# Optimization experiments

Hardware: AMD Instinct MI355X
Metric: run time of the kernel (lower is better)

Reference implementation:

```python
import jax, jax.numpy as jnp
import numpy as np
from jax import lax

TAU_REF_HOURS = 1.0
INIT_NOISE_SCALE = 0.01
MAX_GROWTH_RATE = 0.3
B, T, N, D = 2, 64, 512, 256


def setup_inputs() -> dict:
    key = jax.random.key(0)
    ks = jax.random.split(key, 8)
    return {
        "x": jax.random.normal(ks[0], (B, T, N, D), dtype=jnp.float32),
        "dt": jax.random.uniform(ks[1], (B, T), dtype=jnp.float32),
        "eps": jax.random.normal(ks[2], (B, T, N, D), dtype=jnp.float32),
        "u_raw_re": jax.random.normal(ks[3], (D, D), dtype=jnp.float32) * 0.02,
        "u_raw_im": jax.random.normal(ks[4], (D, D), dtype=jnp.float32) * 0.02,
        "lam_re": jax.random.normal(ks[5], (D,), dtype=jnp.float32) * 0.01,
        "lam_im": jax.random.normal(ks[6], (D,), dtype=jnp.float32) * 0.1,
        "noise_raw": jax.random.normal(ks[7], (D,), dtype=jnp.float32) * 0.02,
    }


def reference(x, dt, eps, u_raw_re, u_raw_im, lam_re, lam_im, noise_raw):
    # Unitary basis from QR of complex raw matrix (ComplexSVDTransform._unitary_from_raw)
    u, _ = jnp.linalg.qr(lax.complex(u_raw_re, u_raw_im))  # [D, D] complex

    # encode: x @ conj(u)
    x_enc = jnp.einsum("btnd,de->btne", x.astype(jnp.complex64), jnp.conj(u))

    # effective lambda: lam_re -> -softplus(-lam_re), clamped at -max_growth_rate
    lam_r = jnp.maximum(-jax.nn.softplus(-lam_re), -MAX_GROWTH_RATE)
    lam = lax.complex(lam_r, lam_im)  # [D]

    # continuous decay / forcing operators per (b, t, d)
    exp_arg = (dt / TAU_REF_HOURS)[..., None] * lam  # [B, T, D]
    decay = jnp.exp(exp_arg)
    lam_safe = lam + (1e-8 * jnp.sign(lam_r + 1e-12)).astype(lam.dtype)
    forcing = (decay - 1.0) / lam_safe  # expm1(arg)/lam_safe

    # SDE noise: eps * sqrt(dt) * softplus(noise_raw) * init_noise_scale
    dt_scale = jnp.sqrt(jnp.maximum(dt, 0.0))[:, :, None, None]  # [B,T,1,1]
    n_scale = jax.nn.softplus(noise_raw) * INIT_NOISE_SCALE  # [D]
    noise = eps.astype(jnp.complex64) * (dt_scale * n_scale).astype(jnp.complex64)

    # linear recurrence h_t = decay_t * h_{t-1} + forcing_t * x_enc_t + noise_t
    b_term = forcing[:, :, None, :] * x_enc + noise  # [B,T,N,D]
    a_term = jnp.broadcast_to(decay[:, :, None, :], b_term.shape)

    def combine(e1, e2):
        a1, b1 = e1
        a2, b2 = e2
        return (a2 * a1, a2 * b1 + b2)

    _, h = lax.associative_scan(combine, (a_term, b_term), axis=1)  # [B,T,N,D]

    # decode: h @ u
    y = jnp.einsum("btnd,de->btne", h, u)
    return jnp.stack([y.real, y.imag])  # [2,B,T,N,D] float32
```

## Files before the change

### kernel.cpp

```cpp
#include <hip/hip_runtime.h>
#include <math.h>

#define B_ 2
#define T_ 64
#define N_ 512
#define D_ 256
#define M_ (B_*T_*N_)
#define PLANE ((size_t)M_*D_)

typedef unsigned short u16;
typedef __attribute__((ext_vector_type(8))) short bf16x8;
typedef __attribute__((ext_vector_type(4))) float f32x4;

__device__ __forceinline__ u16 f2bf(float f) {
  union { float f; unsigned u; } cv; cv.f = f;
  unsigned u = cv.u;
  return (u16)((u + 0x7FFFu + ((u >> 16) & 1u)) >> 16);
}
__device__ __forceinline__ float bf2f(u16 h) {
  union { unsigned u; float f; } cv; cv.u = ((unsigned)h) << 16;
  return cv.f;
}

__device__ __forceinline__ float wredsum(float x) {
  x += __uint_as_float(__builtin_amdgcn_update_dpp(0u, __float_as_uint(x), 0x111, 0xf, 0xf, true));
  x += __uint_as_float(__builtin_amdgcn_update_dpp(0u, __float_as_uint(x), 0x112, 0xf, 0xf, true));
  x += __uint_as_float(__builtin_amdgcn_update_dpp(0u, __float_as_uint(x), 0x114, 0xf, 0xf, true));
  x += __uint_as_float(__builtin_amdgcn_update_dpp(0u, __float_as_uint(x), 0x118, 0xf, 0xf, true));
  x += __uint_as_float(__builtin_amdgcn_update_dpp(0u, __float_as_uint(x), 0x142, 0xa, 0xf, true));
  x += __uint_as_float(__builtin_amdgcn_update_dpp(0u, __float_as_uint(x), 0x143, 0xc, 0xf, true));
  return __uint_as_float(__builtin_amdgcn_readlane(__float_as_uint(x), 63));
}
__device__ __forceinline__ float lanebcast(float x, int l) {
  return __uint_as_float(__builtin_amdgcn_readlane(__float_as_uint(x), l));
}

template<int P>
__global__ __launch_bounds__(1024, 1) void qr_megastep(
    const float* __restrict__ ure_raw, const float* __restrict__ uim_raw,
    float2* __restrict__ A, float2* __restrict__ tau)
{
  const int tid = threadIdx.x, lane = tid & 63, w = tid >> 6;
  const int role = blockIdx.x;
  __shared__ float2 sv32[32][256];
  __shared__ float2 sfin[32][256];
  __shared__ float2 snA[2][256];
  __shared__ float2 snB[2][256];
  __shared__ float4 sscalAB[2];
  __shared__ float2 sg[2];
  __shared__ float2 sgp[16];
  __shared__ float2 stau32[32];
  __shared__ float2 stauOut[32];

  constexpr int J0P  = (P > 0) ? 32*(P-1) : 0;
  constexpr int RP   = 256 - J0P;
  constexpr int MCHP = (RP + 63) >> 6;
  constexpr int PIV  = (P == 0) ? 0 : 32;
  constexpr int J0W  = (P == 0) ? 0 : J0P;
  constexpr int RW   = 256 - J0W;
  constexpr int MCHW = (RW + 63) >> 6;

  if constexpr (P == 0) {
    if (role > 0) {
      const int c0 = 32*role;
      const int c = tid & 31, r0 = tid >> 5;
      #pragma unroll
      for (int r8 = 0; r8 < 8; ++r8) {
        int r = r0 + r8*32;
        A[(size_t)(c0+c)*D_ + r] = make_float2(ure_raw[(size_t)r*D_ + c0 + c],
                                               uim_raw[(size_t)r*D_ + c0 + c]);
      }
      return;
    }
  }

  float2 col[2][4];

  if constexpr (P > 0) {
    #pragma unroll
    for (int it = 0; it < 8; ++it) {
      int idx = it*1024 + tid;
      int c = idx >> 8, rr = idx & 255;
      float2 val = make_float2(0.f, 0.f);
      if (rr < RP) val = A[(size_t)(J0P+c)*D_ + J0P + rr];
      sv32[c][rr] = val;
    }
    if (tid < 32) stau32[tid] = tau[J0P + tid];
    const int c0 = (role > 0) ? 32*(P + role) : 32*P;
    #pragma unroll
    for (int lc = 0; lc < 2; ++lc) {
      int cg = c0 + 2*w + lc;
      #pragma unroll
      for (int m = 0; m < 4; ++m) {
        int rr = m*64 + lane;
        col[lc][m] = make_float2(0.f, 0.f);
        if (m < MCHP && rr < RP) col[lc][m] = A[(size_t)cg*D_ + J0P + rr];
      }
    }
    __syncthreads();

    {
      const int ja = 2*w, jb = 2*w + 1;
      float2 va[4], vb[4];
      { float2 rv = sv32[ja][lane];
        va[0] = (lane > ja) ? rv : ((lane == ja) ? make_float2(1.f, 0.f)
                                                 : make_float2(0.f, 0.f)); }
      { float2 rv = sv32[jb][lane];
        vb[0] = (lane > jb) ? rv : ((lane == jb) ? make_float2(1.f, 0.f)
                                                 : make_float2(0.f, 0.f)); }
      #pragma unroll
      for (int m = 1; m < 4; ++m) { va[m] = sv32[ja][m*64 + lane];
                                    vb[m] = sv32[jb][m*64 + lane]; }
      float gr = 0.f, gi = 0.f;
      #pragma unroll
      for (int m = 0; m < 4; ++m) {
        if (m < MCHP) {
          gr += vb[m].x*va[m].x + vb[m].y*va[m].y;
          gi += vb[m].x*va[m].y - vb[m].y*va[m].x;
        }
      }
      gr = wredsum(gr); gi = wredsum(gi);
      if (lane == 0) sgp[w] = make_float2(gr, gi);
    }
    __syncthreads();

    #pragma unroll 2
    for (int m = 0; m < 16; ++m) {
      const int ja = 2*m, jb = 2*m + 1;
      float2 tA = stau32[ja], tB = stau32[jb];
      float2 g = sgp[m];
      float2 vA[4], vB[4];
      { float2 rv = sv32[ja][lane];
        vA[0] = (lane > ja) ? rv : ((lane == ja) ? make_float2(1.f, 0.f)
                                                 : make_float2(0.f, 0.f)); }
      { float2 rv = sv32[jb][lane];
        vB[0] = (lane > jb) ? rv : ((lane == jb) ? make_float2(1.f, 0.f)
                                                 : make_float2(0.f, 0.f)); }
      #pragma unroll
      for (int mm = 1; mm < 4; ++mm) { vA[mm] = sv32[ja][mm*64 + lane];
                                       vB[mm] = sv32[jb][mm*64 + lane]; }
      #pragma unroll
      for (int lc = 0; lc < 2; ++lc) {
        float d1r = 0.f, d1i = 0.f, d2r = 0.f, d2i = 0.f;
        #pragma unroll
        for (int mm = 0; mm < 4; ++mm) {
          if (mm < MCHP) {
            float2 a = col[lc][mm];
            d1r += vA[mm].x*a.x + vA[mm].y*a.y;
            d1i += vA[mm].x*a.y - vA[mm].y*a.x;
            d2r += vB[mm].x*a.x + vB[mm].y*a.y;
            d2i += vB[mm].x*a.y - vB[mm].y*a.x;
          }
        }
        d1r = wredsum(d1r); d1i = wredsum(d1i);
        d2r = wredsum(d2r); d2i = wredsum(d2i);
        float f1r = tA.x*d1r + tA.y*d1i;
        float f1i = tA.x*d1i - tA.y*d1r;
        float d2cr = d2r - (f1r*g.x - f1i*g.y);
        float d2ci = d2i - (f1r*g.y + f1i*g.x);
        float f2r = tB.x*d2cr + tB.y*d2ci;
        float f2i = tB.x*d2ci - tB.y*d2cr;
        #pragma unroll
        for (int mm = 0; mm < 4; ++mm) {
          if (mm < MCHP) {
            col[lc][mm].x -= f1r*vA[mm].x - f1i*vA[mm].y
                           + f2r*vB[mm].x - f2i*vB[mm].y;
            col[lc][mm].y -= f1r*vA[mm].y + f1i*vA[mm].x
                           + f2r*vB[mm].y + f2i*vB[mm].x;
          }
        }
      }
    }

    if (role > 0) {
      #pragma unroll
      for (int lc = 0; lc < 2; ++lc) {
        int cg = 32*(P + role) + 2*w + lc;
        #pragma unroll
        for (int m = 0; m < 4; ++m) {
          int rr = m*64 + lane;
          if (m < MCHP && rr < RP) A[(size_t)cg*D_ + J0P + rr] = col[lc][m];
        }
      }
      return;
    }
    __syncthreads();
  } else {
    #pragma unroll
    for (int lc = 0; lc < 2; ++lc) {
      int cg = 2*w + lc;
      #pragma unroll
      for (int m = 0; m < 4; ++m) {
        int rr = m*64 + lane;
        col[lc][m] = make_float2(ure_raw[(size_t)rr*D_ + cg],
                                 uim_raw[(size_t)rr*D_ + cg]);
      }
    }
  }

  auto derive_pair = [&](float2 (&ca)[4], float2 (&cb)[4], int jlA, int buf) {
    const int prA = PIV + jlA, prB = prA + 1;
    float part = (lane > prA) ? (ca[0].x*ca[0].x + ca[0].y*ca[0].y) : 0.f;
    if (1 < MCHW) part += ca[1].x*ca[1].x + ca[1].y*ca[1].y;
    if (2 < MCHW) part += ca[2].x*ca[2].x + ca[2].y*ca[2].y;
    if (3 < MCHW) part += ca[3].x*ca[3].x + ca[3].y*ca[3].y;
    part = wredsum(part);
    float ar = lanebcast(ca[0].x, prA), ai = lanebcast(ca[0].y, prA);
    float trA, tiA, sr, si, btA;
    if (part == 0.f && ai == 0.f) {
      trA = tiA = sr = si = 0.f; btA = ar;
    } else {
      float nrm = sqrtf(ar*ar + ai*ai + part);
      btA = (ar >= 0.f) ? -nrm : nrm;
      trA = (btA - ar)/btA; tiA = -ai/btA;
      float dr = ar - btA, di = ai, dn = dr*dr + di*di;
      sr = dr/dn; si = -di/dn;
    }
    float2 vA[4];
    {
      float2 t0 = make_float2(ca[0].x*sr - ca[0].y*si, ca[0].x*si + ca[0].y*sr);
      vA[0] = (lane > prA) ? t0 : ((lane == prA) ? make_float2(1.f, 0.f)
                                                 : make_float2(0.f, 0.f));
    }
    vA[1] = make_float2(ca[1].x*sr - ca[1].y*si, ca[1].x*si + ca[1].y*sr);
    vA[2] = make_float2(ca[2].x*sr - ca[2].y*si, ca[2].x*si + ca[2].y*sr);
    vA[3] = make_float2(ca[3].x*sr - ca[3].y*si, ca[3].x*si + ca[3].y*sr);
    {
      float2 o0 = (lane < prA) ? ca[0]
                : ((lane == prA) ? make_float2(btA, 0.f) : vA[0]);
      sfin[jlA][lane] = o0;
      if (1 < MCHW) sfin[jlA][64 + lane]  = vA[1];
      if (2 < MCHW) sfin[jlA][128 + lane] = vA[2];
      if (3 < MCHW) sfin[jlA][192 + lane] = vA[3];
    }
    {
      float wr_ = vA[0].x*cb[0].x + vA[0].y*cb[0].y;
      float wi_ = vA[0].x*cb[0].y - vA[0].y*cb[0].x;
      if (1 < MCHW) { wr_ += vA[1].x*cb[1].x + vA[1].y*cb[1].y;
                      wi_ += vA[1].x*cb[1].y - vA[1].y*cb[1].x; }
      if (2 < MCHW) { wr_ += vA[2].x*cb[2].x + vA[2].y*cb[2].y;
                      wi_ += vA[2].x*cb[2].y - vA[2].y*cb[2].x; }
      if (3 < MCHW) { wr_ += vA[3].x*cb[3].x + vA[3].y*cb[3].y;
                      wi_ += vA[3].x*cb[3].y - vA[3].y*cb[3].x; }
      wr_ = wredsum(wr_); wi_ = wredsum(wi_);
      float fr = trA*wr_ + tiA*wi_;
      float fi = trA*wi_ - tiA*wr_;
      cb[0].x -= fr*vA[0].x - fi*vA[0].y; cb[0].y -= fr*vA[0].y + fi*vA[0].x;
      if (1 < MCHW) { cb[1].x -= fr*vA[1].x - fi*vA[1].y;
                      cb[1].y -= fr*vA[1].y + fi*vA[1].x; }
      if (2 < MCHW) { cb[2].x -= fr*vA[2].x - fi*vA[2].y;
                      cb[2].y -= fr*vA[2].y + fi*vA[2].x; }
      if (3 < MCHW) { cb[3].x -= fr*vA[3].x - fi*vA[3].y;
                      cb[3].y -= fr*vA[3].y + fi*vA[3].x; }
    }
    float partB = (lane > prB) ? (cb[0].x*cb[0].x + cb[0].y*cb[0].y) : 0.f;
    if (1 < MCHW) partB += cb[1].x*cb[1].x + cb[1].y*cb[1].y;
    if (2 < MCHW) partB += cb[2].x*cb[2].x + cb[2].y*cb[2].y;
    if (3 < MCHW) partB += cb[3].x*cb[3].x + cb[3].y*cb[3].y;
    partB = wredsum(partB);
    float br_ = lanebcast(cb[0].x, prB), bi_ = lanebcast(cb[0].y, prB);
    float trB, tiB, srB, siB, btB;
    if (partB == 0.f && bi_ == 0.f) {
      trB = tiB = srB = siB = 0.f; btB = br_;
    } else {
      float nrm = sqrtf(br_*br_ + bi_*bi_ + partB);
      btB = (br_ >= 0.f) ? -nrm : nrm;
      trB = (btB - br_)/btB; tiB = -bi_/btB;
      float dr = br_ - btB, di = bi_, dn = dr*dr + di*di;
      srB = dr/dn; siB = -di/dn;
    }
    float2 vB[4];
    {
      float2 t0 = make_float2(cb[0].x*srB - cb[0].y*siB, cb[0].x*siB + cb[0].y*srB);
      vB[0] = (lane > prB) ? t0 : ((lane == prB) ? make_float2(1.f, 0.f)
                                                 : make_float2(0.f, 0.f));
    }
    vB[1] = make_float2(cb[1].x*srB - cb[1].y*siB, cb[1].x*siB + cb[1].y*srB);
    vB[2] = make_float2(cb[2].x*srB - cb[2].y*siB, cb[2].x*siB + cb[2].y*srB);
    vB[3] = make_float2(cb[3].x*srB - cb[3].y*siB, cb[3].x*siB + cb[3].y*srB);
    {
      float2 o0 = (lane < prB) ? cb[0]
                : ((lane == prB) ? make_float2(btB, 0.f) : vB[0]);
      sfin[jlA+1][lane] = o0;
      if (1 < MCHW) sfin[jlA+1][64 + lane]  = vB[1];
      if (2 < MCHW) sfin[jlA+1][128 + lane] = vB[2];
      if (3 < MCHW) sfin[jlA+1][192 + lane] = vB[3];
    }
    float gr = vB[0].x*vA[0].x + vB[0].y*vA[0].y;
    float gi = vB[0].x*vA[0].y - vB[0].y*vA[0].x;
    if (1 < MCHW) { gr += vB[1].x*vA[1].x + vB[1].y*vA[1].y;
                    gi += vB[1].x*vA[1].y - vB[1].y*vA[1].x; }
    if (2 < MCHW) { gr += vB[2].x*vA[2].x + vB[2].y*vA[2].y;
                    gi += vB[2].x*vA[2].y - vB[2].y*vA[2].x; }
    if (3 < MCHW) { gr += vB[3].x*vA[3].x + vB[3].y*vA[3].y;
                    gi += vB[3].x*vA[3].y - vB[3].y*vA[3].x; }
    gr = wredsum(gr); gi = wredsum(gi);
    snA[buf][lane] = vA[0]; snA[buf][64+lane] = vA[1];
    snA[buf][128+lane] = vA[2]; snA[buf][192+lane] = vA[3];
    snB[buf][lane] = vB[0]; snB[buf][64+lane] = vB[1];
    snB[buf][128+lane] = vB[2]; snB[buf][192+lane] = vB[3];
    if (lane == 0) {
      sscalAB[buf] = make_float4(trA, tiA, trB, tiB);
      sg[buf] = make_float2(gr, gi);
      stauOut[jlA]   = make_float2(trA, tiA);
      stauOut[jlA+1] = make_float2(trB, tiB);
    }
  };

  if (w == 0) derive_pair(col[0], col[1], 0, 0);
  __syncthreads();

  #pragma unroll 1
  for (int m = 0; m < 15; ++m) {
    const int cur = m & 1, nxt = cur ^ 1;
    float2 vA0 = snA[cur][lane],       vA1 = snA[cur][64 + lane],
           vA2 = snA[cur][128 + lane], vA3 = snA[cur][192 + lane];
    float2 vB0 = snB[cur][lane],       vB1 = snB[cur][64 + lane],
           vB2 = snB[cur][128 + lane], vB3 = snB[cur][192 + lane];
    float4 sc = sscalAB[cur];
    float2 g  = sg[cur];
    #pragma unroll
    for (int lc = 0; lc < 2; ++lc) {
      int cl = 2*w + lc;
      if (cl > 2*m + 1) {
        float d1r, d1i, d2r, d2i;
        { float2 a = col[lc][0];
          d1r = vA0.x*a.x + vA0.y*a.y; d1i = vA0.x*a.y - vA0.y*a.x;
          d2r = vB0.x*a.x + vB0.y*a.y; d2i = vB0.x*a.y - vB0.y*a.x; }
        if (1 < MCHW) { float2 a = col[lc][1];
          d1r += vA1.x*a.x + vA1.y*a.y; d1i += vA1.x*a.y - vA1.y*a.x;
          d2r += vB1.x*a.x + vB1.y*a.y; d2i += vB1.x*a.y - vB1.y*a.x; }
        if (2 < MCHW) { float2 a = col[lc][2];
          d1r += vA2.x*a.x + vA2.y*a.y; d1i += vA2.x*a.y - vA2.y*a.x;
          d2r += vB2.x*a.x + vB2.y*a.y; d2i += vB2.x*a.y - vB2.y*a.x; }
        if (3 < MCHW) { float2 a = col[lc][3];
          d1r += vA3.x*a.x + vA3.y*a.y; d1i += vA3.x*a.y - vA3.y*a.x;
          d2r += vB3.x*a.x + vB3.y*a.y; d2i += vB3.x*a.y - vB3.y*a.x; }
        d1r = wredsum(d1r); d1i = wredsum(d1i);
        d2r = wredsum(d2r); d2i = wredsum(d2i);
        float f1r = sc.x*d1r + sc.y*d1i;
        float f1i = sc.x*d1i - sc.y*d1r;
        float d2cr = d2r - (f1r*g.x - f1i*g.y);
        float d2ci = d2i - (f1r*g.y + f1i*g.x);
        float f2r = sc.z*d2cr + sc.w*d2ci;
        float f2i = sc.z*d2ci - sc.w*d2cr;
        { col[lc][0].x -= f1r*vA0.x - f1i*vA0.y + f2r*vB0.x - f2i*vB0.y;
          col[lc][0].y -= f1r*vA0.y + f1i*vA0.x + f2r*vB0.y + f2i*vB0.x; }
        if (1 < MCHW) {
          col[lc][1].x -= f1r*vA1.x - f1i*vA1.y + f2r*vB1.x - f2i*vB1.y;
          col[lc][1].y -= f1r*vA1.y + f1i*vA1.x + f2r*vB1.y + f2i*vB1.x; }
        if (2 < MCHW) {
          col[lc][2].x -= f1r*vA2.x - f1i*vA2.y + f2r*vB2.x - f2i*vB2.y;
          col[lc][2].y -= f1r*vA2.y + f1i*vA2.x + f2r*vB2.y + f2i*vB2.x; }
        if (3 < MCHW) {
          col[lc][3].x -= f1r*vA3.x - f1i*vA3.y + f2r*vB3.x - f2i*vB3.y;
          col[lc][3].y -= f1r*vA3.y + f1i*vA3.x + f2r*vB3.y + f2i*vB3.x; }
      }
    }
    if (w == m + 1) derive_pair(col[0], col[1], 2*m + 2, nxt);
    __syncthreads();
  }

  #pragma unroll
  for (int it = 0; it < 8; ++it) {
    int idx = it*1024 + tid;
    int c = idx >> 8, rr = idx & 255;
    if (rr < RW) A[(size_t)(32*P + c)*D_ + J0W + rr] = sfin[c][rr];
  }
  if (tid < 32) tau[32*P + tid] = stauOut[tid];
}

__global__ __launch_bounds__(256, 1) void qr_bwd_kernel(
    const float2* __restrict__ A, const float2* __restrict__ tau,
    u16* __restrict__ Benc, u16* __restrict__ Bdec)
{
  const int lane = threadIdx.x & 63;
  const int w = threadIdx.x >> 6;
  const int c = blockIdx.x * 4 + w;
  __shared__ float2 stau[256];
  if (threadIdx.x < 256) stau[threadIdx.x] = tau[threadIdx.x];
  __syncthreads();

  float2 q[4];
  #pragma unroll
  for (int m = 0; m < 4; ++m) {
    q[m] = make_float2(0.f, 0.f);
    if (m*64 + lane == c) q[m].x = 1.f;
  }
  float2 A0[4], A1[4], A2[4], A3[4];
  {
    int i0 = c, i1 = (c >= 1) ? c-1 : 0, i2 = (c >= 2) ? c-2 : 0,
        i3 = (c >= 3) ? c-3 : 0;
    #pragma unroll
    for (int m = 0; m < 4; ++m) {
      A0[m] = A[(size_t)i0*D_ + m*64 + lane];
      A1[m] = A[(size_t)i1*D_ + m*64 + lane];
      A2[m] = A[(size_t)i2*D_ + m*64 + lane];
      A3[m] = A[(size_t)i3*D_ + m*64 + lane];
    }
  }

  int i = c;
  #pragma unroll 1
  while (i >= 1) {
    float2 ta = stau[i], tb = stau[i-1];
    float2 vI[4], vJ[4];
    #pragma unroll
    for (int m = 0; m < 4; ++m) {
      int r = m*64 + lane;
      vI[m] = (r > i)   ? A0[m] : ((r == i)   ? make_float2(1.f, 0.f)
                                              : make_float2(0.f, 0.f));
      vJ[m] = (r > i-1) ? A1[m] : ((r == i-1) ? make_float2(1.f, 0.f)
                                              : make_float2(0.f, 0.f));
    }
    float2 P0[4], P1[4];
    {
      int n0 = (i >= 4) ? i-4 : 0, n1 = (i >= 5) ? i-5 : 0;
      #pragma unroll
      for (int m = 0; m < 4; ++m) {
        P0[m] = A[(size_t)n0*D_ + m*64 + lane];
        P1[m] = A[(size_t)n1*D_ + m*64 + lane];
      }
    }
    float d1r = 0.f, d1i = 0.f, d2r = 0.f, d2i = 0.f, gr = 0.f, gi = 0.f;
    #pragma unroll
    for (int m = 0; m < 4; ++m) {
      d1r += vI[m].x*q[m].x + vI[m].y*q[m].y;
      d1i += vI[m].x*q[m].y - vI[m].y*q[m].x;
      d2r += vJ[m].x*q[m].x + vJ[m].y*q[m].y;
      d2i += vJ[m].x*q[m].y - vJ[m].y*q[m].x;
      gr  += vJ[m].x*vI[m].x + vJ[m].y*vI[m].y;
      gi  += vJ[m].x*vI[m].y - vJ[m].y*vI[m].x;
    }
    d1r = wredsum(d1r); d1i = wredsum(d1i);
    d2r = wredsum(d2r); d2i = wredsum(d2i);
    gr  = wredsum(gr);  gi  = wredsum(gi);
    float f1r = ta.x*d1r - ta.y*d1i;
    float f1i = ta.x*d1i + ta.y*d1r;
    float d2cr = d2r - (f1r*gr - f1i*gi);
    float d2ci = d2i - (f1r*gi + f1i*gr);
    float f2r = tb.x*d2cr - tb.y*d2ci;
    float f2i = tb.x*d2ci + tb.y*d2cr;
    #pragma unroll
    for (int m = 0; m < 4; ++m) {
      q[m].x -= f1r*vI[m].x - f1i*vI[m].y + f2r*vJ[m].x - f2i*vJ[m].y;
      q[m].y -= f1r*vI[m].y + f1i*vI[m].x + f2r*vJ[m].y + f2i*vJ[m].x;
      A0[m] = A2[m]; A1[m] = A3[m]; A2[m] = P0[m]; A3[m] = P1[m];
    }
    i -= 2;
  }
  if (i == 0) {
    float2 tt = stau[0];
    float2 v0[4];
    #pragma unroll
    for (int m = 0; m < 4; ++m) {
      int r = m*64 + lane;
      v0[m] = (r > 0) ? A0[m] : make_float2(1.f, 0.f);
    }
    float wr = 0.f, wi = 0.f;
    #pragma unroll
    for (int m = 0; m < 4; ++m) {
      wr += v0[m].x*q[m].x + v0[m].y*q[m].y;
      wi += v0[m].x*q[m].y - v0[m].y*q[m].x;
    }
    wr = wredsum(wr); wi = wredsum(wi);
    float fr = tt.x*wr - tt.y*wi;
    float fi = tt.x*wi + tt.y*wr;
    #pragma unroll
    for (int m = 0; m < 4; ++m) {
      q[m].x -= fr*v0[m].x - fi*v0[m].y;
      q[m].y -= fr*v0[m].y + fi*v0[m].x;
    }
  }

  #pragma unroll
  for (int m = 0; m < 4; ++m) {
    int r = m*64 + lane;
    u16 qre = f2bf(q[m].x), qim = f2bf(q[m].y), qimn = f2bf(-q[m].y);
    Benc[(size_t)c*D_ + r]              = qre;
    Benc[(size_t)(c+256)*D_ + r]        = qim;
    Bdec[(size_t)c*512 + r]             = qre;
    Bdec[(size_t)c*512 + 256 + r]       = qimn;
    Bdec[(size_t)(c+256)*512 + r]       = qim;
    Bdec[(size_t)(c+256)*512 + 256 + r] = qre;
  }
}

__global__ __launch_bounds__(256) void coef_kernel(
  const float* __restrict__ dt, const float* __restrict__ lam_re, const float* __restrict__ lam_im,
  const float* __restrict__ noise_raw,
  float* __restrict__ c_dre, float* __restrict__ c_dim, float* __restrict__ c_fre,
  float* __restrict__ c_fim, float* __restrict__ c_ns)
{
  int bt = blockIdx.x; int d = threadIdx.x;
  float dtv = dt[bt];
  float lr = lam_re[d], li = lam_im[d];
  float lam_r = fmaxf(-log1pf(expf(-lr)), -0.3f);
  float ar = dtv*lam_r, ai = dtv*li;
  float er = expf(ar);
  float dre = er*cosf(ai), dim_ = er*sinf(ai);
  float t = lam_r + 1e-12f;
  float sgn = (t > 0.f) ? 1.f : ((t < 0.f) ? -1.f : 0.f);
  float den_re = lam_r + 1e-8f*sgn, den_im = li;
  float nr = dre - 1.f, ni = dim_;
  float d2 = den_re*den_re + den_im*den_im;
  float fre = (nr*den_re + ni*den_im)/d2;
  float fim = (ni*den_re - nr*den_im)/d2;
  float ns = sqrtf(fmaxf(dtv,0.f)) * log1pf(expf(noise_raw[d])) * 0.01f;
  int idx = bt*D_+d;
  c_dre[idx]=dre; c_dim[idx]=dim_; c_fre[idx]=fre; c_fim[idx]=fim; c_ns[idx]=ns;
}

#define LDT 72

__device__ __forceinline__ void gemm_tile_idx(int bid, int& m0, int& n0) {
  int ml = bid & 7, t = bid >> 3;
  int n = t & 3, mg = t >> 2;
  m0 = (mg*8 + ml)*128;
  n0 = n*128;
}

__global__ __launch_bounds__(256) void encode_gemm(
    const float* __restrict__ x, const u16* __restrict__ Bt,
    u16* __restrict__ xer16, u16* __restrict__ xei16)
{
  __shared__ u16 sA[128*LDT];
  __shared__ u16 sB[128*LDT];
  const int tid = threadIdx.x;
  const int lane = tid & 63, w = tid >> 6;
  const int wr = w >> 1, wc = w & 1;
  const int l15 = lane & 15, l4 = lane >> 4;
  int m0, n0;
  gemm_tile_idx(blockIdx.x, m0, n0);
  f32x4 acc[4][4] = {};
  for (int kb = 0; kb < 4; ++kb) {
    #pragma unroll
    for (int i = 0; i < 4; ++i) {
      int chunk = i*256 + tid;
      int row = chunk >> 3, k0 = (chunk & 7) * 8;
      const float* xs = x + (size_t)(m0+row)*D_ + kb*64 + k0;
      float4 f0 = *(const float4*)xs;
      float4 f1 = *(const float4*)(xs + 4);
      int4 va;
      va.x = (int)((unsigned)f2bf(f0.x) | ((unsigned)f2bf(f0.y) << 16));
      va.y = (int)((unsigned)f2bf(f0.z) | ((unsigned)f2bf(f0.w) << 16));
      va.z = (int)((unsigned)f2bf(f1.x) | ((unsigned)f2bf(f1.y) << 16));
      va.w = (int)((unsigned)f2bf(f1.z) | ((unsigned)f2bf(f1.w) << 16));
      int4 vb = *(const int4*)(Bt + (size_t)(n0+row)*D_ + kb*64 + k0);
      *(int4*)&sA[row*LDT + k0] = va;
      *(int4*)&sB[row*LDT + k0] = vb;
    }
    __syncthreads();
    #pragma unroll
    for (int ks = 0; ks < 2; ++ks) {
      bf16x8 af[4], bb[4];
      #pragma unroll
      for (int mf = 0; mf < 4; ++mf)
        af[mf] = *(const bf16x8*)&sA[(wr*64 + mf*16 + l15)*LDT + ks*32 + l4*8];
      #pragma unroll
      for (int nf = 0; nf < 4; ++nf)
        bb[nf] = *(const bf16x8*)&sB[(wc*64 + nf*16 + l15)*LDT + ks*32 + l4*8];
      #pragma unroll
      for (int mf = 0; mf < 4; ++mf)
        #pragma unroll
        for (int nf = 0; nf < 4; ++nf)
          acc[mf][nf] = __builtin_amdgcn_mfma_f32_16x16x32_bf16(
              af[mf], bb[nf], acc[mf][nf], 0, 0, 0);
    }
    __syncthreads();
  }
  #pragma unroll
  for (int mf = 0; mf < 4; ++mf)
    #pragma unroll
    for (int nf = 0; nf < 4; ++nf)
      #pragma unroll
      for (int r = 0; r < 4; ++r) {
        int row = m0 + wr*64 + mf*16 + l4*4 + r;
        int col = n0 + wc*64 + nf*16 + l15;
        float v = acc[mf][nf][r];
        if (col < 256) xer16[(size_t)row*D_ + col] = f2bf(v);
        else           xei16[(size_t)row*D_ + col - 256] = f2bf(-v);
      }
}

__global__ __launch_bounds__(256) void decode_gemm(
    const u16* __restrict__ hre16, const u16* __restrict__ him16,
    const u16* __restrict__ Bt, float* __restrict__ out)
{
  __shared__ u16 sA[128*LDT];
  __shared__ u16 sB[128*LDT];
  const int tid = threadIdx.x;
  const int lane = tid & 63, w = tid >> 6;
  const int wr = w >> 1, wc = w & 1;
  const int l15 = lane & 15, l4 = lane >> 4;
  int m0, n0;
  gemm_tile_idx(blockIdx.x, m0, n0);
  f32x4 acc[4][4] = {};
  for (int kb = 0; kb < 8; ++kb) {
    const u16* aplane = (kb < 4) ? hre16 : him16;
    const int kk = (kb & 3) * 64;
    #pragma unroll
    for (int i = 0; i < 4; ++i) {
      int chunk = i*256 + tid;
      int row = chunk >> 3, k0 = (chunk & 7) * 8;
      int4 va = *(const int4*)(aplane + (size_t)(m0+row)*D_ + kk + k0);
      int4 vb = *(const int4*)(Bt + (size_t)(n0+row)*512 + kb*64 + k0);
      *(int4*)&sA[row*LDT + k0] = va;
      *(int4*)&sB[row*LDT + k0] = vb;
    }
    __syncthreads();
    #pragma unroll
    for (int ks = 0; ks < 2; ++ks) {
      bf16x8 af[4], bb[4];
      #pragma unroll
      for (int mf = 0; mf < 4; ++mf)
        af[mf] = *(const bf16x8*)&sA[(wr*64 + mf*16 + l15)*LDT + ks*32 + l4*8];
      #pragma unroll
      for (int nf = 0; nf < 4; ++nf)
        bb[nf] = *(const bf16x8*)&sB[(wc*64 + nf*16 + l15)*LDT + ks*32 + l4*8];
      #pragma unroll
      for (int mf = 0; mf < 4; ++mf)
        #pragma unroll
        for (int nf = 0; nf < 4; ++nf)
          acc[mf][nf] = __builtin_amdgcn_mfma_f32_16x16x32_bf16(
              af[mf], bb[nf], acc[mf][nf], 0, 0, 0);
    }
    __syncthreads();
  }
  #pragma unroll
  for (int mf = 0; mf < 4; ++mf)
    #pragma unroll
    for (int nf = 0; nf < 4; ++nf)
      #pragma unroll
      for (int r = 0; r < 4; ++r) {
        int row = m0 + wr*64 + mf*16 + l4*4 + r;
        int col = n0 + wc*64 + nf*16 + l15;
        float v = acc[mf][nf][r];
        if (col < 256) out[(size_t)row*D_ + col] = v;
        else           out[PLANE + (size_t)row*D_ + col - 256] = v;
      }
}

__global__ __launch_bounds__(256) void scan_kernel(
  const float* __restrict__ eps,
  const float* __restrict__ c_dre, const float* __restrict__ c_dim,
  const float* __restrict__ c_fre, const float* __restrict__ c_fim, const float* __restrict__ c_ns,
  const u16* __restrict__ xer16, const u16* __restrict__ xei16,
  u16* __restrict__ hre16, u16* __restrict__ him16)
{
  int bx = blockIdx.x;
  int b = bx >> 9, n = bx & 511;
  int d = threadIdx.x;
  float hr = 0.f, hi = 0.f;
  for (int t = 0; t < T_; ++t) {
    int bt = b*T_ + t;
    int cidx = bt*D_ + d;
    float dre = c_dre[cidx], dim_ = c_dim[cidx];
    float fre = c_fre[cidx], fim = c_fim[cidx];
    float ns  = c_ns[cidx];
    size_t idx = ((size_t)bt*N_ + n)*D_ + d;
    float xr = bf2f(xer16[idx]), xi = bf2f(xei16[idx]), ep = eps[idx];
    float br = fre*xr - fim*xi + ep*ns;
    float bi = fre*xi + fim*xr;
    float nr2 = dre*hr - dim_*hi + br;
    float ni2 = dre*hi + dim_*hr + bi;
    hr = nr2; hi = ni2;
    hre16[idx] = f2bf(hr); him16[idx] = f2bf(hi);
  }
}

extern "C" void kernel_launch(void* const* d_in, const int* in_sizes, int n_in,
                              void* d_out, int out_size, void* d_ws, size_t ws_size,
                              hipStream_t stream)
{
  const float* x         = (const float*)d_in[0];
  const float* dt        = (const float*)d_in[1];
  const float* eps       = (const float*)d_in[2];
  const float* ure_raw   = (const float*)d_in[3];
  const float* uim_raw   = (const float*)d_in[4];
  const float* lam_re    = (const float*)d_in[5];
  const float* lam_im    = (const float*)d_in[6];
  const float* noise_raw = (const float*)d_in[7];
  float* out = (float*)d_out;

  char* ws = (char*)d_ws;
  float2* A    = (float2*)(ws);
  float2* tau  = (float2*)(ws + 524288);
  u16* Benc    = (u16*)(ws + (1<<20));
  u16* Bdec    = (u16*)(ws + 1572864);
  float* c_dre = (float*)(ws + (2<<20));
  float* c_dim = c_dre + B_*T_*D_;
  float* c_fre = c_dim + B_*T_*D_;
  float* c_fim = c_fre + B_*T_*D_;
  float* c_ns  = c_fim + B_*T_*D_;
  u16* hre16   = (u16*)(ws + ((size_t)4<<20));
  u16* xer16   = (u16*)(ws + ((size_t)36<<20));
  u16* xei16   = (u16*)(ws + ((size_t)68<<20));
  u16* him16   = (u16*)(ws + ((size_t)100<<20));

  qr_megastep<0><<<8, 1024, 0, stream>>>(ure_raw, uim_raw, A, tau);
  qr_megastep<1><<<7, 1024, 0, stream>>>(ure_raw, uim_raw, A, tau);
  qr_megastep<2><<<6, 1024, 0, stream>>>(ure_raw, uim_raw, A, tau);
  qr_megastep<3><<<5, 1024, 0, stream>>>(ure_raw, uim_raw, A, tau);
  qr_megastep<4><<<4, 1024, 0, stream>>>(ure_raw, uim_raw, A, tau);
  qr_megastep<5><<<3, 1024, 0, stream>>>(ure_raw, uim_raw, A, tau);
  qr_megastep<6><<<2, 1024, 0, stream>>>(ure_raw, uim_raw, A, tau);
  qr_megastep<7><<<1, 1024, 0, stream>>>(ure_raw, uim_raw, A, tau);
  qr_bwd_kernel<<<64, 256, 0, stream>>>(A, tau, Benc, Bdec);
  coef_kernel<<<B_*T_, 256, 0, stream>>>(dt, lam_re, lam_im, noise_raw,
                                         c_dre, c_dim, c_fre, c_fim, c_ns);
  encode_gemm<<<2048, 256, 0, stream>>>(x, Benc, xer16, xei16);
  scan_kernel<<<B_*N_, 256, 0, stream>>>(eps, c_dre, c_dim, c_fre, c_fim, c_ns,
                                         xer16, xei16, hre16, him16);
  decode_gemm<<<2048, 256, 0, stream>>>(hre16, him16, Bdec, out);
}
```

Before: 712.1 us.

## Fuse eight QR megastep launches into one kernel with grid barriers

Replaces the eight sequential qr_megastep launches with a single persistent kernel of 8 blocks. The blocks synchronise through a global atomic-counter barrier between panel steps, and a tiny init kernel resets the counter first. This removes per-launch overhead and launch gaps on the serial QR chain. It relies on all 8 blocks being co-resident. Blocks that have no role in a later step skip that body but must still reach every barrier.

```diff
diff --git a/kernel.cpp b/kernel.cpp
--- a/kernel.cpp
+++ b/kernel.cpp
@@ -36,22 +36,15 @@
 }
 
 template<int P>
-__global__ __launch_bounds__(1024, 1) void qr_megastep(
+__device__ __forceinline__ void megastep_body(
+    int role, int tid, int lane, int w,
     const float* __restrict__ ure_raw, const float* __restrict__ uim_raw,
-    float2* __restrict__ A, float2* __restrict__ tau)
+    float2* __restrict__ A, float2* __restrict__ tau,
+    float2 (*sv32)[256], float2 (*sfin)[256],
+    float2 (*snA)[256], float2 (*snB)[256],
+    float4* sscalAB, float2* sg, float2* sgp,
+    float2* stau32, float2* stauOut)
 {
-  const int tid = threadIdx.x, lane = tid & 63, w = tid >> 6;
-  const int role = blockIdx.x;
-  __shared__ float2 sv32[32][256];
-  __shared__ float2 sfin[32][256];
-  __shared__ float2 snA[2][256];
-  __shared__ float2 snB[2][256];
-  __shared__ float4 sscalAB[2];
-  __shared__ float2 sg[2];
-  __shared__ float2 sgp[16];
-  __shared__ float2 stau32[32];
-  __shared__ float2 stauOut[32];
-
   constexpr int J0P  = (P > 0) ? 32*(P-1) : 0;
   constexpr int RP   = 256 - J0P;
   constexpr int MCHP = (RP + 63) >> 6;
@@ -59,6 +52,9 @@
   constexpr int J0W  = (P == 0) ? 0 : J0P;
   constexpr int RW   = 256 - J0W;
   constexpr int MCHW = (RW + 63) >> 6;
+  constexpr int NB   = (P == 0) ? 8 : (8 - P);
+
+  if (role >= NB) return;
 
   if constexpr (P == 0) {
     if (role > 0) {
@@ -370,6 +366,62 @@
   if (tid < 32) tau[32*P + tid] = stauOut[tid];
 }
 
+__device__ __forceinline__ void grid_bar(unsigned* bar, int phase) {
+  __syncthreads();
+  if (threadIdx.x == 0) {
+    __threadfence();
+    atomicAdd(bar, 1u);
+    unsigned target = 8u * (unsigned)(phase + 1);
+    while (__hip_atomic_load(bar, __ATOMIC_ACQUIRE,
+                             __HIP_MEMORY_SCOPE_AGENT) < target) { }
+    __threadfence();
+  }
+  __syncthreads();
+}
+
+__global__ __launch_bounds__(1024, 1) void qr_fused(
+    const float* __restrict__ ure_raw, const float* __restrict__ uim_raw,
+    float2* __restrict__ A, float2* __restrict__ tau, unsigned* __restrict__ bar)
+{
+  const int tid = threadIdx.x, lane = tid & 63, w = tid >> 6;
+  const int role = blockIdx.x;
+  __shared__ float2 sv32[32][256];
+  __shared__ float2 sfin[32][256];
+  __shared__ float2 snA[2][256];
+  __shared__ float2 snB[2][256];
+  __shared__ float4 sscalAB[2];
+  __shared__ float2 sg[2];
+  __shared__ float2 sgp[16];
+  __shared__ float2 stau32[32];
+  __shared__ float2 stauOut[32];
+
+  megastep_body<0>(role, tid, lane, w, ure_raw, uim_raw, A, tau,
+                   sv32, sfin, snA, snB, sscalAB, sg, sgp, stau32, stauOut);
+  grid_bar(bar, 0);
+  megastep_body<1>(role, tid, lane, w, ure_raw, uim_raw, A, tau,
+                   sv32, sfin, snA, snB, sscalAB, sg, sgp, stau32, stauOut);
+  grid_bar(bar, 1);
+  megastep_body<2>(role, tid, lane, w, ure_raw, uim_raw, A, tau,
+                   sv32, sfin, snA, snB, sscalAB, sg, sgp, stau32, stauOut);
+  grid_bar(bar, 2);
+  megastep_body<3>(role, tid, lane, w, ure_raw, uim_raw, A, tau,
+                   sv32, sfin, snA, snB, sscalAB, sg, sgp, stau32, stauOut);
+  grid_bar(bar, 3);
+  megastep_body<4>(role, tid, lane, w, ure_raw, uim_raw, A, tau,
+                   sv32, sfin, snA, snB, sscalAB, sg, sgp, stau32, stauOut);
+  grid_bar(bar, 4);
+  megastep_body<5>(role, tid, lane, w, ure_raw, uim_raw, A, tau,
+                   sv32, sfin, snA, snB, sscalAB, sg, sgp, stau32, stauOut);
+  grid_bar(bar, 5);
+  megastep_body<6>(role, tid, lane, w, ure_raw, uim_raw, A, tau,
+                   sv32, sfin, snA, snB, sscalAB, sg, sgp, stau32, stauOut);
+  grid_bar(bar, 6);
+  megastep_body<7>(role, tid, lane, w, ure_raw, uim_raw, A, tau,
+                   sv32, sfin, snA, snB, sscalAB, sg, sgp, stau32, stauOut);
+}
+
+__global__ void init_bar(unsigned* bar) { *bar = 0u; }
+
 __global__ __launch_bounds__(256, 1) void qr_bwd_kernel(
     const float2* __restrict__ A, const float2* __restrict__ tau,
     u16* __restrict__ Benc, u16* __restrict__ Bdec)
@@ -686,6 +738,7 @@
   char* ws = (char*)d_ws;
   float2* A    = (float2*)(ws);
   float2* tau  = (float2*)(ws + 524288);
+  unsigned* bar = (unsigned*)(ws + 983040);
   u16* Benc    = (u16*)(ws + (1<<20));
   u16* Bdec    = (u16*)(ws + 1572864);
   float* c_dre = (float*)(ws + (2<<20));
@@ -698,14 +751,8 @@
   u16* xei16   = (u16*)(ws + ((size_t)68<<20));
   u16* him16   = (u16*)(ws + ((size_t)100<<20));
 
-  qr_megastep<0><<<8, 1024, 0, stream>>>(ure_raw, uim_raw, A, tau);
-  qr_megastep<1><<<7, 1024, 0, stream>>>(ure_raw, uim_raw, A, tau);
-  qr_megastep<2><<<6, 1024, 0, stream>>>(ure_raw, uim_raw, A, tau);
-  qr_megastep<3><<<5, 1024, 0, stream>>>(ure_raw, uim_raw, A, tau);
-  qr_megastep<4><<<4, 1024, 0, stream>>>(ure_raw, uim_raw, A, tau);
-  qr_megastep<5><<<3, 1024, 0, stream>>>(ure_raw, uim_raw, A, tau);
-  qr_megastep<6><<<2, 1024, 0, stream>>>(ure_raw, uim_raw, A, tau);
-  qr_megastep<7><<<1, 1024, 0, stream>>>(ure_raw, uim_raw, A, tau);
+  init_bar<<<1, 1, 0, stream>>>(bar);
+  qr_fused<<<8, 1024, 0, stream>>>(ure_raw, uim_raw, A, tau, bar);
   qr_bwd_kernel<<<64, 256, 0, stream>>>(A, tau, Benc, Bdec);
   coef_kernel<<<B_*T_, 256, 0, stream>>>(dt, lam_re, lam_im, noise_raw,
                                          c_dre, c_dim, c_fre, c_fim, c_ns);
```

Result: no change. 719.4 us (+1.0%).
